# Kernel tuning notes

Hardware: AMD Instinct MI355X
Metric: run time of the kernel (lower is better)

Reference implementation:

```python
import jax, jax.numpy as jnp
import numpy as np

D_MODEL = 768
NUM_HEADS = 12
DEPTH = D_MODEL // NUM_HEADS


def setup_inputs() -> dict:
    key = jax.random.key(0)
    ks = jax.random.split(key, 11)
    B, S, D = 2, 2048, D_MODEL
    scale = 1.0 / np.sqrt(D)
    inp = {
        "v": jax.random.normal(ks[0], (B, S, D), jnp.float32),
        "k": jax.random.normal(ks[1], (B, S, D), jnp.float32),
        "q": jax.random.normal(ks[2], (B, S, D), jnp.float32),
        "wq": jax.random.normal(ks[3], (D, D), jnp.float32) * scale,
        "bq": jnp.zeros((D,), jnp.float32),
        "wk": jax.random.normal(ks[4], (D, D), jnp.float32) * scale,
        "bk": jnp.zeros((D,), jnp.float32),
        "wv": jax.random.normal(ks[5], (D, D), jnp.float32) * scale,
        "bv": jnp.zeros((D,), jnp.float32),
        "wo": jax.random.normal(ks[6], (D, D), jnp.float32) * scale,
        "bo": jnp.zeros((D,), jnp.float32),
    }
    return inp


def _split_heads(x):
    # (B, S, D) -> (B, H, S, depth)
    B, S, _ = x.shape
    return x.reshape(B, S, NUM_HEADS, DEPTH).transpose(0, 2, 1, 3)


def reference(v, k, q, wq, bq, wk, bk, wv, bv, wo, bo):
    B, S, D = q.shape
    qh = _split_heads(q @ wq + bq)  # (B,H,S,dh)
    kh = _split_heads(k @ wk + bk)
    vh = _split_heads(v @ wv + bv)
    logits = jnp.einsum("bhqd,bhkd->bhqk", qh, kh) / jnp.sqrt(
        jnp.asarray(DEPTH, qh.dtype)
    )
    attn = jax.nn.softmax(logits, axis=-1)  # (B,H,S,S)
    ctx = jnp.einsum("bhqk,bhkd->bhqd", attn, vh)
    ctx = ctx.transpose(0, 2, 1, 3).reshape(B, S, D)
    return ctx @ wo + bo
```

## Files before the change

### kernel.cpp

```cpp
#include <hip/hip_runtime.h>
#include <hip/hip_bf16.h>
#include <math.h>

typedef __bf16 bf16;
typedef __attribute__((ext_vector_type(8))) __bf16 bf16x8;
typedef __attribute__((ext_vector_type(4))) __bf16 bf16x4v;
typedef __attribute__((ext_vector_type(4))) float f32x4;
typedef __attribute__((ext_vector_type(2))) unsigned int u32x2;

#define MFMA16(a, b, c) __builtin_amdgcn_mfma_f32_16x16x32_bf16(a, b, c, 0, 0, 0)

__device__ __forceinline__ void gld16(const bf16* g, bf16* l) {
  __builtin_amdgcn_global_load_lds((const __attribute__((address_space(1))) void*)g,
                                   (__attribute__((address_space(3))) void*)l, 16, 0, 0);
}

__device__ __forceinline__ unsigned int pkbf(float a, float b) {
  union { unsigned int u; __bf16 h[2]; } r;
  r.h[0] = (bf16)a;
  r.h[1] = (bf16)b;
  return r.u;
}

__global__ __launch_bounds__(256) void prep(const float* __restrict__ q,
                                            const float* __restrict__ k,
                                            const float* __restrict__ v,
                                            bf16* __restrict__ qb, bf16* __restrict__ kb,
                                            bf16* __restrict__ vb,
                                            const float* __restrict__ w0,
                                            const float* __restrict__ w1,
                                            const float* __restrict__ w2,
                                            const float* __restrict__ w3,
                                            bf16* __restrict__ t0, bf16* __restrict__ t1,
                                            bf16* __restrict__ t2, bf16* __restrict__ t3) {
  const int lin = blockIdx.x;
  if (lin < 4608) {
    const int which = lin / 1536, idx = lin % 1536;
    const float* a = which == 0 ? q : (which == 1 ? k : v);
    bf16* o = which == 0 ? qb : (which == 1 ? kb : vb);
    const size_t i = ((size_t)idx * 256 + threadIdx.x) * 8;
    const float4 f0 = *(const float4*)(a + i);
    const float4 f1 = *(const float4*)(a + i + 4);
    bf16x8 r = {(bf16)f0.x, (bf16)f0.y, (bf16)f0.z, (bf16)f0.w,
                (bf16)f1.x, (bf16)f1.y, (bf16)f1.z, (bf16)f1.w};
    *(bf16x8*)(o + i) = r;
  } else {
    const int w = lin - 4608;
    const int z = w / 576, rem = w % 576;
    const int by = rem / 24, bx = rem % 24;
    const float* W = z == 0 ? w0 : (z == 1 ? w1 : (z == 2 ? w2 : w3));
    bf16* T = z == 0 ? t0 : (z == 1 ? t1 : (z == 2 ? t2 : t3));
    __shared__ float t[32][33];
    const int tx = threadIdx.x & 31, ty = threadIdx.x >> 5;
    const int c0 = bx * 32, r0 = by * 32;
#pragma unroll
    for (int i = 0; i < 4; ++i) {
      const int r = ty + 8 * i;
      t[r][tx] = W[(size_t)(r0 + r) * 768 + c0 + tx];
    }
    __syncthreads();
#pragma unroll
    for (int i = 0; i < 4; ++i) {
      const int r = ty + 8 * i;
      T[(size_t)(c0 + r) * 768 + r0 + tx] = (bf16)t[tx][r];
    }
  }
}

__device__ __forceinline__ void gemm_core(const bf16* __restrict__ A, const bf16* __restrict__ BT,
                                          int row0, int col0, bf16* As, bf16* Bs,
                                          f32x4 acc[4][4]) {
  const int tid = threadIdx.x;
  const int lane = tid & 63, wave = tid >> 6;
  const int m15 = lane & 15, kg = lane >> 4;
  const int wm = wave >> 1, wn = wave & 1;
  const int pr16 = lane & 15;
  const int pk8 = (lane >> 4) * 8;
#pragma unroll
  for (int i = 0; i < 4; ++i)
#pragma unroll
    for (int j = 0; j < 4; ++j) acc[i][j] = f32x4{0.f, 0.f, 0.f, 0.f};

  for (int k0 = 0; k0 < 768; k0 += 32) {
#pragma unroll
    for (int j = 0; j < 2; ++j) {
      const int i = wave * 2 + j;
      gld16(A + (size_t)(row0 + 16 * i + pr16) * 768 + k0 + pk8, As + i * 512);
      gld16(BT + (size_t)(col0 + 16 * i + pr16) * 768 + k0 + pk8, Bs + i * 512);
    }
    __syncthreads();
    bf16x8 af[4], bfr[4];
#pragma unroll
    for (int t = 0; t < 4; ++t)
      af[t] = *(const bf16x8*)(As + (4 * wm + t) * 512 + kg * 128 + m15 * 8);
#pragma unroll
    for (int t = 0; t < 4; ++t)
      bfr[t] = *(const bf16x8*)(Bs + (4 * wn + t) * 512 + kg * 128 + m15 * 8);
#pragma unroll
    for (int mt = 0; mt < 4; ++mt)
#pragma unroll
      for (int nt = 0; nt < 4; ++nt) acc[mt][nt] = MFMA16(af[mt], bfr[nt], acc[mt][nt]);
    __syncthreads();
  }
}

__global__ __launch_bounds__(256, 3) void gemm_qkv(
    const bf16* __restrict__ qb, const bf16* __restrict__ kb, const bf16* __restrict__ vb,
    const bf16* __restrict__ wqT, const bf16* __restrict__ wkT, const bf16* __restrict__ wvT,
    const float* __restrict__ bq, const float* __restrict__ bk, const float* __restrict__ bv,
    bf16* __restrict__ Qh, bf16* __restrict__ Kh, bf16* __restrict__ Vt) {
  __shared__ bf16 As[128 * 32], Bs[128 * 32];
  const bf16 *A, *BT;
  const float* bias;
  bf16* out;
  int mode;
  if (blockIdx.z == 0) { A = qb; BT = wqT; bias = bq; out = Qh; mode = 0; }
  else if (blockIdx.z == 1) { A = kb; BT = wkT; bias = bk; out = Kh; mode = 0; }
  else { A = vb; BT = wvT; bias = bv; out = Vt; mode = 1; }
  const int row0 = blockIdx.y * 128, col0 = blockIdx.x * 128;
  f32x4 acc[4][4];
  gemm_core(A, BT, row0, col0, As, Bs, acc);

  const int lane = threadIdx.x & 63, wave = threadIdx.x >> 6;
  const int m15 = lane & 15, kg = lane >> 4;
  const int wm = wave >> 1, wn = wave & 1;
#pragma unroll
  for (int mt = 0; mt < 4; ++mt) {
#pragma unroll
    for (int nt = 0; nt < 4; ++nt) {
      const int col = col0 + 64 * wn + 16 * nt + m15;
      const float bb = bias[col];
      const int h = col >> 6, d = col & 63;
      const int rowb = row0 + 64 * wm + 16 * mt + kg * 4;
      const int b = rowb >> 11, s0 = rowb & 2047;
      if (mode == 0) {
#pragma unroll
        for (int r = 0; r < 4; ++r)
          out[((size_t)(b * 12 + h) * 2048 + s0 + r) * 64 + d] = (bf16)(acc[mt][nt][r] + bb);
      } else {
        bf16x4v pk;
#pragma unroll
        for (int r = 0; r < 4; ++r) pk[r] = (bf16)(acc[mt][nt][r] + bb);
        *(bf16x4v*)&out[((size_t)(b * 12 + h) * 64 + d) * 2048 + s0] = pk;
      }
    }
  }
}

__global__ __launch_bounds__(256, 3) void gemm_out(const bf16* __restrict__ A,
                                                   const bf16* __restrict__ BT,
                                                   const float* __restrict__ bias,
                                                   float* __restrict__ out) {
  __shared__ bf16 As[128 * 32], Bs[128 * 32];
  const int row0 = blockIdx.y * 128, col0 = blockIdx.x * 128;
  f32x4 acc[4][4];
  gemm_core(A, BT, row0, col0, As, Bs, acc);

  const int lane = threadIdx.x & 63, wave = threadIdx.x >> 6;
  const int m15 = lane & 15, kg = lane >> 4;
  const int wm = wave >> 1, wn = wave & 1;
#pragma unroll
  for (int mt = 0; mt < 4; ++mt) {
#pragma unroll
    for (int nt = 0; nt < 4; ++nt) {
      const int col = col0 + 64 * wn + 16 * nt + m15;
      const float bb = bias[col];
      const int rowb = row0 + 64 * wm + 16 * mt + kg * 4;
#pragma unroll
      for (int r = 0; r < 4; ++r)
        out[(size_t)(rowb + r) * 768 + col] = acc[mt][nt][r] + bb;
    }
  }
}

__global__ __launch_bounds__(256, 3) void attn_kernel(const bf16* __restrict__ Q,
                                                      const bf16* __restrict__ K,
                                                      const bf16* __restrict__ VT,
                                                      bf16* __restrict__ ctx) {
  __shared__ __align__(16) bf16 S[21504];

  const int tid = threadIdx.x;
  const int lane = tid & 63, wave = tid >> 6;
  const int m15 = lane & 15, kg = lane >> 4;
  const int lin = blockIdx.x;
  const int bh = lin % 24, qblk = lin / 24;
  const size_t hb = (size_t)bh * 2048 * 64;
  const bf16* Qp = Q + hb;
  const bf16* Kp = K + hb;
  const bf16* Vp = VT + hb;
  const int pipe = wave >> 1;
  const int qrow0 = qblk * 64 + (wave & 1) * 32;
  bf16* Pw = S + 16384 + wave * 1280;

  const int kpr = lane & 7, kpc = (lane >> 3) * 8;
  const int vpr = lane & 15, vpc = (lane >> 4) * 8;

  bf16x8 qf[2][2];
#pragma unroll
  for (int t = 0; t < 2; ++t)
#pragma unroll
    for (int ks = 0; ks < 2; ++ks) {
      bf16x8 tv = *(const bf16x8*)&Qp[(size_t)(qrow0 + 16 * t + m15) * 64 + 32 * ks + kg * 8];
#pragma unroll
      for (int j = 0; j < 8; ++j) tv[j] = (bf16)((float)tv[j] * 0.125f);
      qf[t][ks] = tv;
    }

  f32x4 o[2][4];
  float lpq[2];
#pragma unroll
  for (int t = 0; t < 2; ++t) {
#pragma unroll
    for (int nt = 0; nt < 4; ++nt) o[t][nt] = f32x4{0.f, 0.f, 0.f, 0.f};
    lpq[t] = 0.f;
  }

#pragma unroll
  for (int j = 0; j < 4; ++j) {
    const int idx = wave * 4 + j;
    const int sp = idx >> 3, r8 = idx & 7;
    const int kc = sp * 1024;
    if (r8 < 4)
      gld16(Kp + (size_t)(kc + 8 * r8 + kpr) * 64 + kpc, S + sp * 2 * 2048 + r8 * 512);
    else {
      const int i = r8 - 4;
      gld16(Vp + (size_t)(16 * i + vpr) * 2048 + kc + vpc, S + 8192 + sp * 2 * 2048 + i * 512);
    }
  }

  for (int c = 0; c < 32; ++c) {
    const int buf = c & 1;
    __syncthreads();
    if (c < 31) {
      const int nb = buf ^ 1;
#pragma unroll
      for (int j = 0; j < 4; ++j) {
        const int idx = wave * 4 + j;
        const int sp = idx >> 3, r8 = idx & 7;
        const int kc = sp * 1024 + (c + 1) * 32;
        if (r8 < 4)
          gld16(Kp + (size_t)(kc + 8 * r8 + kpr) * 64 + kpc,
                S + (sp * 2 + nb) * 2048 + r8 * 512);
        else {
          const int i = r8 - 4;
          gld16(Vp + (size_t)(16 * i + vpr) * 2048 + kc + vpc,
                S + 8192 + (sp * 2 + nb) * 2048 + i * 512);
        }
      }
    }
    const bf16* KsB = S + (pipe * 2 + buf) * 2048;
    const bf16* VsB = S + 8192 + (pipe * 2 + buf) * 2048;

    f32x4 s[2][2];
#pragma unroll
    for (int kt = 0; kt < 2; ++kt)
#pragma unroll
      for (int qt = 0; qt < 2; ++qt) s[kt][qt] = f32x4{0.f, 0.f, 0.f, 0.f};
#pragma unroll
    for (int ks = 0; ks < 2; ++ks) {
#pragma unroll
      for (int kt = 0; kt < 2; ++kt) {
        const int key = 16 * kt + m15;
        const bf16x8 kf =
            *(const bf16x8*)&KsB[(key >> 3) * 512 + (4 * ks + kg) * 64 + (key & 7) * 8];
        s[kt][0] = MFMA16(kf, qf[0][ks], s[kt][0]);
        s[kt][1] = MFMA16(kf, qf[1][ks], s[kt][1]);
      }
    }
#pragma unroll
    for (int kt = 0; kt < 2; ++kt)
#pragma unroll
      for (int qt = 0; qt < 2; ++qt) {
        float pe0 = __expf(s[kt][qt][0]);
        float pe1 = __expf(s[kt][qt][1]);
        float pe2 = __expf(s[kt][qt][2]);
        float pe3 = __expf(s[kt][qt][3]);
        lpq[qt] += (pe0 + pe1) + (pe2 + pe3);
        u32x2 pk;
        pk[0] = pkbf(pe0, pe1);
        pk[1] = pkbf(pe2, pe3);
        *(u32x2*)&Pw[(qt * 16 + m15) * 40 + kt * 16 + kg * 4] = pk;
      }
    asm volatile("s_waitcnt lgkmcnt(0)" ::: "memory");
    const bf16x8 pf0 = *(const bf16x8*)&Pw[(0 * 16 + m15) * 40 + kg * 8];
    const bf16x8 pf1 = *(const bf16x8*)&Pw[(1 * 16 + m15) * 40 + kg * 8];
#pragma unroll
    for (int nt = 0; nt < 4; ++nt) {
      const int d = 16 * nt + m15;
      const bf16x8 vf =
          *(const bf16x8*)&VsB[(d >> 4) * 512 + kg * 128 + (d & 15) * 8];
      o[0][nt] = MFMA16(pf0, vf, o[0][nt]);
      o[1][nt] = MFMA16(pf1, vf, o[1][nt]);
    }
  }

#pragma unroll
  for (int t = 0; t < 2; ++t) {
    lpq[t] += __shfl_xor(lpq[t], 16);
    lpq[t] += __shfl_xor(lpq[t], 32);
  }

  __syncthreads();
  float* sc = (float*)S;
  if (wave >= 2) {
    const int rg = (wave - 2) * 2560;
#pragma unroll
    for (int t = 0; t < 2; ++t)
#pragma unroll
      for (int nt = 0; nt < 4; ++nt)
        *(f32x4*)&sc[rg + (t * 4 + nt) * 256 + lane * 4] = o[t][nt];
    sc[rg + 2048 + lane * 2] = lpq[0];
    sc[rg + 2048 + lane * 2 + 1] = lpq[1];
  }
  __syncthreads();
  if (wave < 2) {
    const int rg = wave * 2560;
#pragma unroll
    for (int t = 0; t < 2; ++t)
#pragma unroll
      for (int nt = 0; nt < 4; ++nt) {
        const f32x4 po = *(const f32x4*)&sc[rg + (t * 4 + nt) * 256 + lane * 4];
#pragma unroll
        for (int j = 0; j < 4; ++j) o[t][nt][j] += po[j];
      }
    lpq[0] += sc[rg + 2048 + lane * 2];
    lpq[1] += sc[rg + 2048 + lane * 2 + 1];
    float lpr[2][4];
#pragma unroll
    for (int t = 0; t < 2; ++t)
#pragma unroll
      for (int r = 0; r < 4; ++r) lpr[t][r] = __shfl(lpq[t], kg * 4 + r);
    const int b = bh / 12, h = bh % 12;
#pragma unroll
    for (int t = 0; t < 2; ++t)
#pragma unroll
      for (int nt = 0; nt < 4; ++nt)
#pragma unroll
        for (int r = 0; r < 4; ++r) {
          const int sr = qrow0 + 16 * t + kg * 4 + r;
          ctx[((size_t)(b * 2048) + sr) * 768 + h * 64 + 16 * nt + m15] =
              (bf16)(o[t][nt][r] / lpr[t][r]);
        }
  }
}

extern "C" void kernel_launch(void* const* d_in, const int* in_sizes, int n_in,
                              void* d_out, int out_size, void* d_ws, size_t ws_size,
                              hipStream_t stream) {
  const float* v = (const float*)d_in[0];
  const float* k = (const float*)d_in[1];
  const float* q = (const float*)d_in[2];
  const float* wq = (const float*)d_in[3];
  const float* bq = (const float*)d_in[4];
  const float* wk = (const float*)d_in[5];
  const float* bk = (const float*)d_in[6];
  const float* wv = (const float*)d_in[7];
  const float* bv = (const float*)d_in[8];
  const float* wo = (const float*)d_in[9];
  const float* bo = (const float*)d_in[10];

  char* ws = (char*)d_ws;
  const size_t SEG = (size_t)4096 * 768 * sizeof(bf16);
  const size_t WSEG = (size_t)768 * 768 * sizeof(bf16);
  bf16* Qh = (bf16*)(ws + 0 * SEG);
  bf16* Kh = (bf16*)(ws + 1 * SEG);
  bf16* Vt = (bf16*)(ws + 2 * SEG);
  bf16* qb = (bf16*)(ws + 3 * SEG);
  bf16* kb = (bf16*)(ws + 4 * SEG);
  bf16* vb = (bf16*)(ws + 5 * SEG);
  bf16* ctx = qb;
  bf16* wqT = (bf16*)(ws + 6 * SEG);
  bf16* wkT = (bf16*)(ws + 6 * SEG + WSEG);
  bf16* wvT = (bf16*)(ws + 6 * SEG + 2 * WSEG);
  bf16* woT = (bf16*)(ws + 6 * SEG + 3 * WSEG);

  prep<<<dim3(6912), 256, 0, stream>>>(q, k, v, qb, kb, vb, wq, wk, wv, wo,
                                       wqT, wkT, wvT, woT);
  gemm_qkv<<<dim3(6, 32, 3), 256, 0, stream>>>(qb, kb, vb, wqT, wkT, wvT, bq, bk, bv,
                                               Qh, Kh, Vt);
  attn_kernel<<<dim3(768), 256, 0, stream>>>(Qh, Kh, Vt, ctx);
  gemm_out<<<dim3(6, 32), 256, 0, stream>>>(ctx, woT, bo, (float*)d_out);
}
```

Baseline: 218.6 us.

## Split attention work across 8 waves with 16 query rows each

The attention block grows from 256 to 512 threads. Each of the 8 waves now handles 16 query rows instead of 32, in two key pipes of four waves, and the K/V tile loads are spread over more waves. The intent is more waves per CU for latency hiding and fewer registers per wave. In exchange, each K/V fragment read from LDS feeds half as many MFMAs, so LDS traffic per FLOP doubles, and block-wide sync costs rise.

```diff
diff --git a/kernel.cpp b/kernel.cpp
--- a/kernel.cpp
+++ b/kernel.cpp
@@ -173,7 +173,7 @@
   }
 }
 
-__global__ __launch_bounds__(256, 3) void attn_kernel(const bf16* __restrict__ Q,
+__global__ __launch_bounds__(512, 6) void attn_kernel(const bf16* __restrict__ Q,
                                                       const bf16* __restrict__ K,
                                                       const bf16* __restrict__ VT,
                                                       bf16* __restrict__ ctx) {
@@ -188,36 +188,30 @@
   const bf16* Qp = Q + hb;
   const bf16* Kp = K + hb;
   const bf16* Vp = VT + hb;
-  const int pipe = wave >> 1;
-  const int qrow0 = qblk * 64 + (wave & 1) * 32;
-  bf16* Pw = S + 16384 + wave * 1280;
+  const int pipe = wave >> 2;
+  const int qrow0 = qblk * 64 + (wave & 3) * 16;
+  bf16* Pw = S + 16384 + wave * 640;
 
   const int kpr = lane & 7, kpc = (lane >> 3) * 8;
   const int vpr = lane & 15, vpc = (lane >> 4) * 8;
 
-  bf16x8 qf[2][2];
-#pragma unroll
-  for (int t = 0; t < 2; ++t)
-#pragma unroll
-    for (int ks = 0; ks < 2; ++ks) {
-      bf16x8 tv = *(const bf16x8*)&Qp[(size_t)(qrow0 + 16 * t + m15) * 64 + 32 * ks + kg * 8];
-#pragma unroll
-      for (int j = 0; j < 8; ++j) tv[j] = (bf16)((float)tv[j] * 0.125f);
-      qf[t][ks] = tv;
-    }
-
-  f32x4 o[2][4];
-  float lpq[2];
-#pragma unroll
-  for (int t = 0; t < 2; ++t) {
-#pragma unroll
-    for (int nt = 0; nt < 4; ++nt) o[t][nt] = f32x4{0.f, 0.f, 0.f, 0.f};
-    lpq[t] = 0.f;
-  }
-
-#pragma unroll
-  for (int j = 0; j < 4; ++j) {
-    const int idx = wave * 4 + j;
+  bf16x8 qf[2];
+#pragma unroll
+  for (int ks = 0; ks < 2; ++ks) {
+    bf16x8 tv = *(const bf16x8*)&Qp[(size_t)(qrow0 + m15) * 64 + 32 * ks + kg * 8];
+#pragma unroll
+    for (int j = 0; j < 8; ++j) tv[j] = (bf16)((float)tv[j] * 0.125f);
+    qf[ks] = tv;
+  }
+
+  f32x4 o[4];
+  float lpq = 0.f;
+#pragma unroll
+  for (int nt = 0; nt < 4; ++nt) o[nt] = f32x4{0.f, 0.f, 0.f, 0.f};
+
+#pragma unroll
+  for (int j = 0; j < 2; ++j) {
+    const int idx = wave * 2 + j;
     const int sp = idx >> 3, r8 = idx & 7;
     const int kc = sp * 1024;
     if (r8 < 4)
@@ -234,8 +228,8 @@
     if (c < 31) {
       const int nb = buf ^ 1;
 #pragma unroll
-      for (int j = 0; j < 4; ++j) {
-        const int idx = wave * 4 + j;
+      for (int j = 0; j < 2; ++j) {
+        const int idx = wave * 2 + j;
         const int sp = idx >> 3, r8 = idx & 7;
         const int kc = sp * 1024 + (c + 1) * 32;
         if (r8 < 4)
@@ -251,11 +245,9 @@
     const bf16* KsB = S + (pipe * 2 + buf) * 2048;
     const bf16* VsB = S + 8192 + (pipe * 2 + buf) * 2048;
 
-    f32x4 s[2][2];
-#pragma unroll
-    for (int kt = 0; kt < 2; ++kt)
-#pragma unroll
-      for (int qt = 0; qt < 2; ++qt) s[kt][qt] = f32x4{0.f, 0.f, 0.f, 0.f};
+    f32x4 s[2];
+#pragma unroll
+    for (int kt = 0; kt < 2; ++kt) s[kt] = f32x4{0.f, 0.f, 0.f, 0.f};
 #pragma unroll
     for (int ks = 0; ks < 2; ++ks) {
 #pragma unroll
@@ -263,84 +255,65 @@
         const int key = 16 * kt + m15;
         const bf16x8 kf =
             *(const bf16x8*)&KsB[(key >> 3) * 512 + (4 * ks + kg) * 64 + (key & 7) * 8];
-        s[kt][0] = MFMA16(kf, qf[0][ks], s[kt][0]);
-        s[kt][1] = MFMA16(kf, qf[1][ks], s[kt][1]);
+        s[kt] = MFMA16(kf, qf[ks], s[kt]);
       }
     }
 #pragma unroll
-    for (int kt = 0; kt < 2; ++kt)
-#pragma unroll
-      for (int qt = 0; qt < 2; ++qt) {
-        float pe0 = __expf(s[kt][qt][0]);
-        float pe1 = __expf(s[kt][qt][1]);
-        float pe2 = __expf(s[kt][qt][2]);
-        float pe3 = __expf(s[kt][qt][3]);
-        lpq[qt] += (pe0 + pe1) + (pe2 + pe3);
-        u32x2 pk;
-        pk[0] = pkbf(pe0, pe1);
-        pk[1] = pkbf(pe2, pe3);
-        *(u32x2*)&Pw[(qt * 16 + m15) * 40 + kt * 16 + kg * 4] = pk;
-      }
+    for (int kt = 0; kt < 2; ++kt) {
+      float pe0 = __expf(s[kt][0]);
+      float pe1 = __expf(s[kt][1]);
+      float pe2 = __expf(s[kt][2]);
+      float pe3 = __expf(s[kt][3]);
+      lpq += (pe0 + pe1) + (pe2 + pe3);
+      u32x2 pk;
+      pk[0] = pkbf(pe0, pe1);
+      pk[1] = pkbf(pe2, pe3);
+      *(u32x2*)&Pw[m15 * 40 + kt * 16 + kg * 4] = pk;
+    }
     asm volatile("s_waitcnt lgkmcnt(0)" ::: "memory");
-    const bf16x8 pf0 = *(const bf16x8*)&Pw[(0 * 16 + m15) * 40 + kg * 8];
-    const bf16x8 pf1 = *(const bf16x8*)&Pw[(1 * 16 + m15) * 40 + kg * 8];
+    const bf16x8 pf = *(const bf16x8*)&Pw[m15 * 40 + kg * 8];
 #pragma unroll
     for (int nt = 0; nt < 4; ++nt) {
       const int d = 16 * nt + m15;
       const bf16x8 vf =
           *(const bf16x8*)&VsB[(d >> 4) * 512 + kg * 128 + (d & 15) * 8];
-      o[0][nt] = MFMA16(pf0, vf, o[0][nt]);
-      o[1][nt] = MFMA16(pf1, vf, o[1][nt]);
-    }
-  }
-
-#pragma unroll
-  for (int t = 0; t < 2; ++t) {
-    lpq[t] += __shfl_xor(lpq[t], 16);
-    lpq[t] += __shfl_xor(lpq[t], 32);
-  }
+      o[nt] = MFMA16(pf, vf, o[nt]);
+    }
+  }
+
+  lpq += __shfl_xor(lpq, 16);
+  lpq += __shfl_xor(lpq, 32);
 
   __syncthreads();
   float* sc = (float*)S;
-  if (wave >= 2) {
-    const int rg = (wave - 2) * 2560;
-#pragma unroll
-    for (int t = 0; t < 2; ++t)
-#pragma unroll
-      for (int nt = 0; nt < 4; ++nt)
-        *(f32x4*)&sc[rg + (t * 4 + nt) * 256 + lane * 4] = o[t][nt];
-    sc[rg + 2048 + lane * 2] = lpq[0];
-    sc[rg + 2048 + lane * 2 + 1] = lpq[1];
+  if (wave >= 4) {
+    const int rg = (wave - 4) * 1088;
+#pragma unroll
+    for (int nt = 0; nt < 4; ++nt) *(f32x4*)&sc[rg + nt * 256 + lane * 4] = o[nt];
+    sc[rg + 1024 + lane] = lpq;
   }
   __syncthreads();
-  if (wave < 2) {
-    const int rg = wave * 2560;
-#pragma unroll
-    for (int t = 0; t < 2; ++t)
-#pragma unroll
-      for (int nt = 0; nt < 4; ++nt) {
-        const f32x4 po = *(const f32x4*)&sc[rg + (t * 4 + nt) * 256 + lane * 4];
-#pragma unroll
-        for (int j = 0; j < 4; ++j) o[t][nt][j] += po[j];
+  if (wave < 4) {
+    const int rg = wave * 1088;
+#pragma unroll
+    for (int nt = 0; nt < 4; ++nt) {
+      const f32x4 po = *(const f32x4*)&sc[rg + nt * 256 + lane * 4];
+#pragma unroll
+      for (int j = 0; j < 4; ++j) o[nt][j] += po[j];
+    }
+    lpq += sc[rg + 1024 + lane];
+    float lpr[4];
+#pragma unroll
+    for (int r = 0; r < 4; ++r) lpr[r] = __shfl(lpq, kg * 4 + r);
+    const int b = bh / 12, h = bh % 12;
+#pragma unroll
+    for (int nt = 0; nt < 4; ++nt)
+#pragma unroll
+      for (int r = 0; r < 4; ++r) {
+        const int sr = qrow0 + kg * 4 + r;
+        ctx[((size_t)(b * 2048) + sr) * 768 + h * 64 + 16 * nt + m15] =
+            (bf16)(o[nt][r] / lpr[r]);
       }
-    lpq[0] += sc[rg + 2048 + lane * 2];
-    lpq[1] += sc[rg + 2048 + lane * 2 + 1];
-    float lpr[2][4];
-#pragma unroll
-    for (int t = 0; t < 2; ++t)
-#pragma unroll
-      for (int r = 0; r < 4; ++r) lpr[t][r] = __shfl(lpq[t], kg * 4 + r);
-    const int b = bh / 12, h = bh % 12;
-#pragma unroll
-    for (int t = 0; t < 2; ++t)
-#pragma unroll
-      for (int nt = 0; nt < 4; ++nt)
-#pragma unroll
-        for (int r = 0; r < 4; ++r) {
-          const int sr = qrow0 + 16 * t + kg * 4 + r;
-          ctx[((size_t)(b * 2048) + sr) * 768 + h * 64 + 16 * nt + m15] =
-              (bf16)(o[t][nt][r] / lpr[t][r]);
-        }
   }
 }
 
@@ -378,6 +351,6 @@
                                        wqT, wkT, wvT, woT);
   gemm_qkv<<<dim3(6, 32, 3), 256, 0, stream>>>(qb, kb, vb, wqT, wkT, wvT, bq, bk, bv,
                                                Qh, Kh, Vt);
-  attn_kernel<<<dim3(768), 256, 0, stream>>>(Qh, Kh, Vt, ctx);
+  attn_kernel<<<dim3(768), 512, 0, stream>>>(Qh, Kh, Vt, ctx);
   gemm_out<<<dim3(6, 32), 256, 0, stream>>>(ctx, woT, bo, (float*)d_out);
 }
```

Result: no change. 217.6 us (-0.4%).
